# Optimization experiments

Measured on AMD Instinct MI355X. Metric: run time of the kernel, lower is better.

Reference implementation:

```python
import jax, jax.numpy as jnp
import numpy as np


def setup_inputs() -> dict:
    key = jax.random.key(0)
    B, R, A, T, S = 16, 1, 16, 14, 1024  # batch, num_rx, num_rx_ant, num_ofdm_symbols, num_eff_subcarriers
    k1, k2 = jax.random.split(key)
    y_real = jax.random.normal(k1, (B, R, A, T, S), dtype=jnp.float32)
    y_imag = jax.random.normal(k2, (B, R, A, T, S), dtype=jnp.float32)

    # Emulate PilotPattern-derived constants (computed in __init__ in the original):
    # zero-power pilot positions at OFDM symbols {2, 11}, every 2nd subcarrier.
    pilot_syms = np.array([2, 11], dtype=np.int64)
    est_sc = np.arange(0, S, 2, dtype=np.int64)  # estimated subcarriers (unique)
    sym_grid, sc_grid = np.meshgrid(pilot_syms, est_sc, indexing='ij')  # row-major like tf.where
    estimation_indices = jnp.asarray(
        np.stack([sym_grid.ravel(), sc_grid.ravel()], axis=1), dtype=jnp.int32)  # [P, 2]
    # Nearest estimated subcarrier for every subcarrier (np.argmin tie -> first, like original).
    closest = est_sc[np.argmin(np.abs(est_sc[None, :] - np.arange(S)[:, None]), axis=1)]
    closest_subcarrier = jnp.asarray(closest, dtype=jnp.int32)  # [S]

    return {"y_real": y_real, "y_imag": y_imag,
            "estimation_indices": estimation_indices,
            "closest_subcarrier": closest_subcarrier}


def reference(y_real, y_imag, estimation_indices, closest_subcarrier):
    y = jax.lax.complex(y_real, y_imag)  # [B,R,A,T,S] complex64
    B, R, A, T, S = y.shape
    sym = estimation_indices[:, 0]
    sc = estimation_indices[:, 1]

    # gather_nd over the (symbol, subcarrier) positions -> [B,R,A,P]
    sig = y[:, :, :, sym, sc]
    # per-position outer product over antennas -> [P,B,R,A,A]
    cov_el = jnp.einsum('brip,brjp->pbrij', sig, jnp.conj(sig))

    # unsorted_segment_mean over subcarrier ids (real/imag separately, as in TF)
    counts = jax.ops.segment_sum(jnp.ones_like(sc, dtype=jnp.float32), sc, num_segments=S)
    denom = jnp.maximum(counts, 1.0)[:, None, None, None, None]  # empty segments -> 0, like TF
    sum_r = jax.ops.segment_sum(cov_el.real, sc, num_segments=S)
    sum_i = jax.ops.segment_sum(cov_el.imag, sc, num_segments=S)
    cov_sw = jax.lax.complex(sum_r / denom, sum_i / denom)  # [S,B,R,A,A]

    # nearest-neighbor interpolation over subcarriers
    cov_nn = cov_sw[closest_subcarrier]                      # [S,B,R,A,A]
    cov = jnp.transpose(cov_nn, (1, 2, 0, 3, 4))             # [B,R,S,A,A]
    cov = cov[:, :, None]                                    # [B,R,1,S,A,A]
    return jnp.broadcast_to(cov, (B, R, T, S, A, A))
```

## Files before the change

kernel.cpp:

```cpp
#include <hip/hip_runtime.h>

static constexpr int kB = 16;
static constexpr int kA = 16;
static constexpr int kT = 14;
static constexpr int kS = 1024;
static constexpr int kMaxMatch = 32;


__global__ __launch_bounds__(64) void cov_real_kernel(
    const float* __restrict__ y_real,
    const float* __restrict__ y_imag,
    const int*   __restrict__ est,
    const int*   __restrict__ closest,
    float*       __restrict__ out,
    int P, long out_floats)
{
    const int blk = blockIdx.x;
    const int b   = blk >> 10;
    const int s   = blk & (kS - 1);
    const int tid = threadIdx.x;

    bool est64 = true;
    {
        int lim = 2 * P; if (lim > 128) lim = 128;
        for (int k = 1; k < lim; k += 2)
            if (est[k] != 0) { est64 = false; break; }
    }
    bool clo64 = true;
    {
        int lim = kS; if (lim > 128) lim = 128;
        for (int k = 1; k < lim; k += 2)
            if (closest[k] != 0) { clo64 = false; break; }
    }

    int c = closest[clo64 ? 2 * s : s];
    if (c < 0) c = 0;
    if (c >= kS) c = kS - 1;

    __shared__ int   sm_count;
    __shared__ int   sm_sym[kMaxMatch];
    __shared__ float sm_re[kA], sm_im[kA];

    if (tid == 0) sm_count = 0;
    __syncthreads();

    for (int p = tid; p < P; p += 64) {
        const int sc = est[est64 ? 4 * p + 2 : 2 * p + 1];
        if (sc == c) {
            const int sym = est[est64 ? 4 * p : 2 * p];
            if (sym >= 0 && sym < kT) {
                int slot = atomicAdd(&sm_count, 1);
                if (slot < kMaxMatch) sm_sym[slot] = sym;
            }
        }
    }
    __syncthreads();

    int count = sm_count;
    if (count > kMaxMatch) count = kMaxMatch;

    const int i  = tid >> 2;
    const int j0 = (tid & 3) * 4;

    float v0 = 0.f, v1 = 0.f, v2 = 0.f, v3 = 0.f;

    for (int m = 0; m < count; ++m) {
        const int sym = sm_sym[m];
        if (tid < kA) {
            const long off = (long)b * (kA * kT * kS) + (long)tid * (kT * kS)
                           + (long)sym * kS + c;
            sm_re[tid] = y_real[off];
            sm_im[tid] = y_imag[off];
        }
        __syncthreads();

        const float xr = sm_re[i], xi = sm_im[i];
        v0 += xr * sm_re[j0 + 0] + xi * sm_im[j0 + 0];
        v1 += xr * sm_re[j0 + 1] + xi * sm_im[j0 + 1];
        v2 += xr * sm_re[j0 + 2] + xi * sm_im[j0 + 2];
        v3 += xr * sm_re[j0 + 3] + xi * sm_im[j0 + 3];
        __syncthreads();
    }

    const float inv = 1.0f / (float)(count > 0 ? count : 1);
    const float4 v = make_float4(v0 * inv, v1 * inv, v2 * inv, v3 * inv);

    float4* __restrict__ out4 = (float4*)out;
    for (int t = 0; t < kT; ++t) {
        const long f4idx = ((long)(b * kT + t) * kS + s) * 64 + tid;
        if ((f4idx + 1) * 4 <= out_floats)
            out4[f4idx] = v;
    }
}

__global__ __launch_bounds__(128) void cov_cplx_kernel(
    const float* __restrict__ y_real,
    const float* __restrict__ y_imag,
    const int*   __restrict__ est,
    const int*   __restrict__ closest,
    float*       __restrict__ out,
    int P, long out_floats)
{
    const int blk = blockIdx.x;
    const int b   = blk >> 10;
    const int s   = blk & (kS - 1);
    const int tid = threadIdx.x;

    bool est64 = true;
    {
        int lim = 2 * P; if (lim > 128) lim = 128;
        for (int k = 1; k < lim; k += 2)
            if (est[k] != 0) { est64 = false; break; }
    }
    bool clo64 = true;
    {
        int lim = kS; if (lim > 128) lim = 128;
        for (int k = 1; k < lim; k += 2)
            if (closest[k] != 0) { clo64 = false; break; }
    }

    int c = closest[clo64 ? 2 * s : s];
    if (c < 0) c = 0;
    if (c >= kS) c = kS - 1;

    __shared__ int   sm_count;
    __shared__ int   sm_sym[kMaxMatch];
    __shared__ float sm_re[kA], sm_im[kA];

    if (tid == 0) sm_count = 0;
    __syncthreads();

    for (int p = tid; p < P; p += 128) {
        const int sc = est[est64 ? 4 * p + 2 : 2 * p + 1];
        if (sc == c) {
            const int sym = est[est64 ? 4 * p : 2 * p];
            if (sym >= 0 && sym < kT) {
                int slot = atomicAdd(&sm_count, 1);
                if (slot < kMaxMatch) sm_sym[slot] = sym;
            }
        }
    }
    __syncthreads();

    int count = sm_count;
    if (count > kMaxMatch) count = kMaxMatch;

    const int i  = tid >> 3;
    const int j0 = (tid & 7) * 2;

    float a0r = 0.f, a0i = 0.f, a1r = 0.f, a1i = 0.f;

    for (int m = 0; m < count; ++m) {
        const int sym = sm_sym[m];
        if (tid < kA) {
            const long off = (long)b * (kA * kT * kS) + (long)tid * (kT * kS)
                           + (long)sym * kS + c;
            sm_re[tid] = y_real[off];
            sm_im[tid] = y_imag[off];
        }
        __syncthreads();

        const float xr  = sm_re[i],      xi  = sm_im[i];
        const float y0r = sm_re[j0],     y0i = sm_im[j0];
        const float y1r = sm_re[j0 + 1], y1i = sm_im[j0 + 1];
        a0r += xr * y0r + xi * y0i;
        a0i += xi * y0r - xr * y0i;
        a1r += xr * y1r + xi * y1i;
        a1i += xi * y1r - xr * y1i;
        __syncthreads();
    }

    const float inv = 1.0f / (float)(count > 0 ? count : 1);
    const float4 v = make_float4(a0r * inv, a0i * inv, a1r * inv, a1i * inv);

    float4* __restrict__ out4 = (float4*)out;
    for (int t = 0; t < kT; ++t) {
        const long f4idx = ((long)(b * kT + t) * kS + s) * 128 + tid;
        if ((f4idx + 1) * 4 <= out_floats)
            out4[f4idx] = v;
    }
}

extern "C" void kernel_launch(void* const* d_in, const int* in_sizes, int n_in,
                              void* d_out, int out_size, void* d_ws, size_t ws_size,
                              hipStream_t stream) {
    const float* y_real  = (const float*)d_in[0];
    const float* y_imag  = (const float*)d_in[1];
    const int*   est     = (const int*)d_in[2];
    const int*   closest = (const int*)d_in[3];
    float*       out     = (float*)d_out;

    const int  P     = in_sizes[2] / 2;
    const long realN = (long)kB * kT * kS * kA * kA;

    dim3 grid(kB * kS);
    if ((long)out_size >= 2 * realN) {
        cov_cplx_kernel<<<grid, dim3(128), 0, stream>>>(
            y_real, y_imag, est, closest, out, P, (long)out_size);
    } else {
        cov_real_kernel<<<grid, dim3(64), 0, stream>>>(
            y_real, y_imag, est, closest, out, P, (long)out_size);
    }
}
```

Before: 266.5 us.

## Split covariance into compute-to-workspace and nontemporal broadcast store kernels

Computes the per-(batch, subcarrier) covariance once into a workspace buffer, then launches a separate broadcast kernel that copies each 8-subcarrier chunk to all OFDM symbols. The broadcast kernel uses nontemporal stores and larger blocks. The aim is to make the roughly 235 MB output write stream more efficiently than the original, which did 14 scattered stores per small block. The cost is an extra kernel launch and a 16 MB workspace write and read, and the new path runs only when the workspace is large enough.

```diff
diff --git a/kernel.cpp b/kernel.cpp
--- a/kernel.cpp
+++ b/kernel.cpp
@@ -6,6 +6,123 @@
 static constexpr int kS = 1024;
 static constexpr int kMaxMatch = 32;
 
+typedef __attribute__((ext_vector_type(4))) float fvec4;
+
+
+__global__ __launch_bounds__(128) void cov_compute_ws(
+    const float* __restrict__ y_real,
+    const float* __restrict__ y_imag,
+    const int*   __restrict__ est,
+    const int*   __restrict__ closest,
+    fvec4*       __restrict__ ws4,
+    int P)
+{
+    const int blk = blockIdx.x;
+    const int b   = blk >> 10;
+    const int s   = blk & (kS - 1);
+    const int tid = threadIdx.x;
+
+    bool est64 = true;
+    {
+        int lim = 2 * P; if (lim > 128) lim = 128;
+        for (int k = 1; k < lim; k += 2)
+            if (est[k] != 0) { est64 = false; break; }
+    }
+    bool clo64 = true;
+    {
+        int lim = kS; if (lim > 128) lim = 128;
+        for (int k = 1; k < lim; k += 2)
+            if (closest[k] != 0) { clo64 = false; break; }
+    }
+
+    int c = closest[clo64 ? 2 * s : s];
+    if (c < 0) c = 0;
+    if (c >= kS) c = kS - 1;
+
+    __shared__ int   sm_count;
+    __shared__ int   sm_sym[kMaxMatch];
+    __shared__ float sm_re[kA], sm_im[kA];
+
+    if (tid == 0) sm_count = 0;
+    __syncthreads();
+
+    for (int p = tid; p < P; p += 128) {
+        const int sc = est[est64 ? 4 * p + 2 : 2 * p + 1];
+        if (sc == c) {
+            const int sym = est[est64 ? 4 * p : 2 * p];
+            if (sym >= 0 && sym < kT) {
+                int slot = atomicAdd(&sm_count, 1);
+                if (slot < kMaxMatch) sm_sym[slot] = sym;
+            }
+        }
+    }
+    __syncthreads();
+
+    int count = sm_count;
+    if (count > kMaxMatch) count = kMaxMatch;
+
+    const int i  = tid >> 3;
+    const int j0 = (tid & 7) * 2;
+
+    float a0r = 0.f, a0i = 0.f, a1r = 0.f, a1i = 0.f;
+
+    for (int m = 0; m < count; ++m) {
+        const int sym = sm_sym[m];
+        if (tid < kA) {
+            const long off = (long)b * (kA * kT * kS) + (long)tid * (kT * kS)
+                           + (long)sym * kS + c;
+            sm_re[tid] = y_real[off];
+            sm_im[tid] = y_imag[off];
+        }
+        __syncthreads();
+
+        const float xr  = sm_re[i],      xi  = sm_im[i];
+        const float y0r = sm_re[j0],     y0i = sm_im[j0];
+        const float y1r = sm_re[j0 + 1], y1i = sm_im[j0 + 1];
+        a0r += xr * y0r + xi * y0i;
+        a0i += xi * y0r - xr * y0i;
+        a1r += xr * y1r + xi * y1i;
+        a1i += xi * y1r - xr * y1i;
+        __syncthreads();
+    }
+
+    const float inv = 1.0f / (float)(count > 0 ? count : 1);
+    fvec4 v; v.x = a0r * inv; v.y = a0i * inv; v.z = a1r * inv; v.w = a1i * inv;
+    ws4[(long)blk * 128 + tid] = v;
+}
+
+__global__ __launch_bounds__(256) void cov_broadcast(
+    const fvec4* __restrict__ ws4,
+    fvec4*       __restrict__ out4,
+    long out_floats)
+{
+    const int b     = blockIdx.x >> 7;
+    const int chunk = blockIdx.x & 127;
+    const int s0    = chunk << 3;
+    const int tid   = threadIdx.x;
+
+    const fvec4* __restrict__ src = ws4 + ((long)((b << 10) + s0)) * 128;
+    const fvec4 r0 = src[tid];
+    const fvec4 r1 = src[tid + 256];
+    const fvec4 r2 = src[tid + 512];
+    const fvec4 r3 = src[tid + 768];
+
+    #pragma unroll
+    for (int t = 0; t < kT; ++t) {
+        const long base = ((long)((b * kT + t) << 10) + s0) * 128;
+        if ((base + 1024) * 4 <= out_floats) {
+            __builtin_nontemporal_store(r0, out4 + base + tid);
+            __builtin_nontemporal_store(r1, out4 + base + tid + 256);
+            __builtin_nontemporal_store(r2, out4 + base + tid + 512);
+            __builtin_nontemporal_store(r3, out4 + base + tid + 768);
+        } else {
+            if ((base + tid + 1)       * 4 <= out_floats) out4[base + tid]       = r0;
+            if ((base + tid + 256 + 1) * 4 <= out_floats) out4[base + tid + 256] = r1;
+            if ((base + tid + 512 + 1) * 4 <= out_floats) out4[base + tid + 512] = r2;
+            if ((base + tid + 768 + 1) * 4 <= out_floats) out4[base + tid + 768] = r3;
+        }
+    }
+}
 
 __global__ __launch_bounds__(64) void cov_real_kernel(
     const float* __restrict__ y_real,
@@ -192,11 +309,20 @@
 
     const int  P     = in_sizes[2] / 2;
     const long realN = (long)kB * kT * kS * kA * kA;
+    const long wsNeed = (long)kB * kS * 128 * 16;
 
     dim3 grid(kB * kS);
     if ((long)out_size >= 2 * realN) {
-        cov_cplx_kernel<<<grid, dim3(128), 0, stream>>>(
-            y_real, y_imag, est, closest, out, P, (long)out_size);
+        if (ws_size >= (size_t)wsNeed) {
+            fvec4* ws4 = (fvec4*)d_ws;
+            cov_compute_ws<<<grid, dim3(128), 0, stream>>>(
+                y_real, y_imag, est, closest, ws4, P);
+            cov_broadcast<<<dim3(kB * (kS / 8)), dim3(256), 0, stream>>>(
+                ws4, (fvec4*)out, (long)out_size);
+        } else {
+            cov_cplx_kernel<<<grid, dim3(128), 0, stream>>>(
+                y_real, y_imag, est, closest, out, P, (long)out_size);
+        }
     } else {
         cov_real_kernel<<<grid, dim3(64), 0, stream>>>(
             y_real, y_imag, est, closest, out, P, (long)out_size);
```

Result: no change. 266.8 us (+0.1%).

## Process eight subcarriers per block with shared-memory staged contiguous nontemporal stores

Applied to the files above, without the earlier changes.

Replaces the per-(batch, subcarrier) complex kernel with a 256-thread block that handles eight consecutive subcarriers. Each warp-row computes one subcarrier's 16x16 complex covariance, and the results are staged in shared memory. Each block then writes contiguous 16 KB chunks per OFDM symbol using nontemporal stores. This cuts the block count by eight and amortises the index-scan prologue, aiming at write bandwidth on the output-bound broadcast. The cost is more shared memory per block and a loop bounded by the row with the most matches.

```diff
diff --git a/kernel.cpp b/kernel.cpp
--- a/kernel.cpp
+++ b/kernel.cpp
@@ -5,7 +5,150 @@
 static constexpr int kT = 14;
 static constexpr int kS = 1024;
 static constexpr int kMaxMatch = 32;
-
+static constexpr int kRows = 8;
+
+typedef __attribute__((ext_vector_type(4))) float fvec4;
+
+
+__global__ __launch_bounds__(256) void cov_fused(
+    const float* __restrict__ y_real,
+    const float* __restrict__ y_imag,
+    const int*   __restrict__ est,
+    const int*   __restrict__ closest,
+    fvec4*       __restrict__ out4,
+    int P, long out_floats)
+{
+    const int b    = blockIdx.x >> 7;
+    const int s0   = (blockIdx.x & 127) << 3;
+    const int tid  = threadIdx.x;
+    const int row  = tid >> 5;
+    const int lane = tid & 31;
+
+    bool est64 = true;
+    {
+        int lim = 2 * P; if (lim > 128) lim = 128;
+        for (int k = 1; k < lim; k += 2)
+            if (est[k] != 0) { est64 = false; break; }
+    }
+    bool clo64 = true;
+    {
+        int lim = kS; if (lim > 128) lim = 128;
+        for (int k = 1; k < lim; k += 2)
+            if (closest[k] != 0) { clo64 = false; break; }
+    }
+
+    __shared__ int   sm_c[kRows];
+    __shared__ int   sm_cnt[kRows];
+    __shared__ int   sm_sym[kRows][kMaxMatch];
+    __shared__ float sm_re[kRows][kA];
+    __shared__ float sm_im[kRows][kA];
+    __shared__ fvec4 sm_out[kRows * 128];
+
+    if (tid < kRows) {
+        const int s = s0 + tid;
+        int c = closest[clo64 ? 2 * s : s];
+        if (c < 0) c = 0;
+        if (c >= kS) c = kS - 1;
+        sm_c[tid]   = c;
+        sm_cnt[tid] = 0;
+    }
+    __syncthreads();
+
+    {
+        const int c = sm_c[row];
+        for (int p = lane; p < P; p += 32) {
+            const int sc = est[est64 ? 4 * p + 2 : 2 * p + 1];
+            if (sc == c) {
+                const int sym = est[est64 ? 4 * p : 2 * p];
+                if (sym >= 0 && sym < kT) {
+                    int slot = atomicAdd(&sm_cnt[row], 1);
+                    if (slot < kMaxMatch) sm_sym[row][slot] = sym;
+                }
+            }
+        }
+    }
+    __syncthreads();
+
+    int cnt = sm_cnt[row]; if (cnt > kMaxMatch) cnt = kMaxMatch;
+    int mmax = 0;
+    #pragma unroll
+    for (int r = 0; r < kRows; ++r) {
+        int cr = sm_cnt[r]; if (cr > kMaxMatch) cr = kMaxMatch;
+        if (cr > mmax) mmax = cr;
+    }
+
+    float acc[16];
+    #pragma unroll
+    for (int k = 0; k < 16; ++k) acc[k] = 0.f;
+
+    const int i = lane >> 1;
+
+    for (int m = 0; m < mmax; ++m) {
+        {
+            const int half = tid >> 7;
+            const int r    = (tid >> 4) & 7;
+            const int a    = tid & 15;
+            int cr = sm_cnt[r]; if (cr > kMaxMatch) cr = kMaxMatch;
+            if (m < cr) {
+                const int sym = sm_sym[r][m];
+                const long off = (long)b * (kA * kT * kS) + (long)a * (kT * kS)
+                               + (long)sym * kS + sm_c[r];
+                if (half == 0) sm_re[r][a] = y_real[off];
+                else           sm_im[r][a] = y_imag[off];
+            }
+        }
+        __syncthreads();
+
+        if (m < cnt) {
+            const float xr = sm_re[row][i], xi = sm_im[row][i];
+            #pragma unroll
+            for (int k = 0; k < 4; ++k) {
+                const int q  = 4 * lane + k;
+                const int j0 = (q & 7) * 2;
+                const float y0r = sm_re[row][j0],     y0i = sm_im[row][j0];
+                const float y1r = sm_re[row][j0 + 1], y1i = sm_im[row][j0 + 1];
+                acc[4 * k + 0] += xr * y0r + xi * y0i;
+                acc[4 * k + 1] += xi * y0r - xr * y0i;
+                acc[4 * k + 2] += xr * y1r + xi * y1i;
+                acc[4 * k + 3] += xi * y1r - xr * y1i;
+            }
+        }
+        __syncthreads();
+    }
+
+    const float inv = 1.0f / (float)(cnt > 0 ? cnt : 1);
+    #pragma unroll
+    for (int k = 0; k < 4; ++k) {
+        fvec4 v;
+        v.x = acc[4 * k + 0] * inv;
+        v.y = acc[4 * k + 1] * inv;
+        v.z = acc[4 * k + 2] * inv;
+        v.w = acc[4 * k + 3] * inv;
+        sm_out[row * 128 + 4 * lane + k] = v;
+    }
+    __syncthreads();
+
+    const fvec4 r0 = sm_out[tid];
+    const fvec4 r1 = sm_out[tid + 256];
+    const fvec4 r2 = sm_out[tid + 512];
+    const fvec4 r3 = sm_out[tid + 768];
+
+    #pragma unroll
+    for (int t = 0; t < kT; ++t) {
+        const long base = ((long)((b * kT + t) << 10) + s0) * 128;
+        if ((base + 1024) * 4 <= out_floats) {
+            __builtin_nontemporal_store(r0, out4 + base + tid);
+            __builtin_nontemporal_store(r1, out4 + base + tid + 256);
+            __builtin_nontemporal_store(r2, out4 + base + tid + 512);
+            __builtin_nontemporal_store(r3, out4 + base + tid + 768);
+        } else {
+            if ((base + tid + 1)       * 4 <= out_floats) out4[base + tid]       = r0;
+            if ((base + tid + 256 + 1) * 4 <= out_floats) out4[base + tid + 256] = r1;
+            if ((base + tid + 512 + 1) * 4 <= out_floats) out4[base + tid + 512] = r2;
+            if ((base + tid + 768 + 1) * 4 <= out_floats) out4[base + tid + 768] = r3;
+        }
+    }
+}
 
 __global__ __launch_bounds__(64) void cov_real_kernel(
     const float* __restrict__ y_real,
@@ -93,94 +236,6 @@
     }
 }
 
-__global__ __launch_bounds__(128) void cov_cplx_kernel(
-    const float* __restrict__ y_real,
-    const float* __restrict__ y_imag,
-    const int*   __restrict__ est,
-    const int*   __restrict__ closest,
-    float*       __restrict__ out,
-    int P, long out_floats)
-{
-    const int blk = blockIdx.x;
-    const int b   = blk >> 10;
-    const int s   = blk & (kS - 1);
-    const int tid = threadIdx.x;
-
-    bool est64 = true;
-    {
-        int lim = 2 * P; if (lim > 128) lim = 128;
-        for (int k = 1; k < lim; k += 2)
-            if (est[k] != 0) { est64 = false; break; }
-    }
-    bool clo64 = true;
-    {
-        int lim = kS; if (lim > 128) lim = 128;
-        for (int k = 1; k < lim; k += 2)
-            if (closest[k] != 0) { clo64 = false; break; }
-    }
-
-    int c = closest[clo64 ? 2 * s : s];
-    if (c < 0) c = 0;
-    if (c >= kS) c = kS - 1;
-
-    __shared__ int   sm_count;
-    __shared__ int   sm_sym[kMaxMatch];
-    __shared__ float sm_re[kA], sm_im[kA];
-
-    if (tid == 0) sm_count = 0;
-    __syncthreads();
-
-    for (int p = tid; p < P; p += 128) {
-        const int sc = est[est64 ? 4 * p + 2 : 2 * p + 1];
-        if (sc == c) {
-            const int sym = est[est64 ? 4 * p : 2 * p];
-            if (sym >= 0 && sym < kT) {
-                int slot = atomicAdd(&sm_count, 1);
-                if (slot < kMaxMatch) sm_sym[slot] = sym;
-            }
-        }
-    }
-    __syncthreads();
-
-    int count = sm_count;
-    if (count > kMaxMatch) count = kMaxMatch;
-
-    const int i  = tid >> 3;
-    const int j0 = (tid & 7) * 2;
-
-    float a0r = 0.f, a0i = 0.f, a1r = 0.f, a1i = 0.f;
-
-    for (int m = 0; m < count; ++m) {
-        const int sym = sm_sym[m];
-        if (tid < kA) {
-            const long off = (long)b * (kA * kT * kS) + (long)tid * (kT * kS)
-                           + (long)sym * kS + c;
-            sm_re[tid] = y_real[off];
-            sm_im[tid] = y_imag[off];
-        }
-        __syncthreads();
-
-        const float xr  = sm_re[i],      xi  = sm_im[i];
-        const float y0r = sm_re[j0],     y0i = sm_im[j0];
-        const float y1r = sm_re[j0 + 1], y1i = sm_im[j0 + 1];
-        a0r += xr * y0r + xi * y0i;
-        a0i += xi * y0r - xr * y0i;
-        a1r += xr * y1r + xi * y1i;
-        a1i += xi * y1r - xr * y1i;
-        __syncthreads();
-    }
-
-    const float inv = 1.0f / (float)(count > 0 ? count : 1);
-    const float4 v = make_float4(a0r * inv, a0i * inv, a1r * inv, a1i * inv);
-
-    float4* __restrict__ out4 = (float4*)out;
-    for (int t = 0; t < kT; ++t) {
-        const long f4idx = ((long)(b * kT + t) * kS + s) * 128 + tid;
-        if ((f4idx + 1) * 4 <= out_floats)
-            out4[f4idx] = v;
-    }
-}
-
 extern "C" void kernel_launch(void* const* d_in, const int* in_sizes, int n_in,
                               void* d_out, int out_size, void* d_ws, size_t ws_size,
                               hipStream_t stream) {
@@ -193,11 +248,11 @@
     const int  P     = in_sizes[2] / 2;
     const long realN = (long)kB * kT * kS * kA * kA;
 
-    dim3 grid(kB * kS);
     if ((long)out_size >= 2 * realN) {
-        cov_cplx_kernel<<<grid, dim3(128), 0, stream>>>(
-            y_real, y_imag, est, closest, out, P, (long)out_size);
+        cov_fused<<<dim3(kB * (kS / kRows)), dim3(256), 0, stream>>>(
+            y_real, y_imag, est, closest, (fvec4*)out, P, (long)out_size);
     } else {
+        dim3 grid(kB * kS);
         cov_real_kernel<<<grid, dim3(64), 0, stream>>>(
             y_real, y_imag, est, closest, out, P, (long)out_size);
     }
```

Result: no change. 264.8 us (-0.6%).

## Precompute pilot match tables and write output linearly per (batch,symbol) block

Applied to the files above, without the earlier changes.

Adds a single-block preprocessing kernel that resolves the nearest-subcarrier map and groups pilot symbols per subcarrier into workspace. The main kernel then launches one block per (batch, symbol, 32-subcarrier chunk), so each block writes one contiguous 64KB region with nontemporal stores. This replaces the old layout where each block wrote 14 strided slices and rescanned the index arrays. In exchange, every block recomputes the covariance for its subcarriers (redundant across the 14 symbols), and there is an extra tiny launch plus a dependency on workspace size.

```diff
diff --git a/kernel.cpp b/kernel.cpp
--- a/kernel.cpp
+++ b/kernel.cpp
@@ -6,6 +6,161 @@
 static constexpr int kS = 1024;
 static constexpr int kMaxMatch = 32;
 
+typedef __attribute__((ext_vector_type(4))) float fvec4;
+
+
+static constexpr long kWsInts = 2048 + (long)kS * kMaxMatch;
+
+__global__ __launch_bounds__(1024) void build_meta(
+    const int* __restrict__ est,
+    const int* __restrict__ closest,
+    int*       __restrict__ wsi,
+    int P)
+{
+    const int tid = threadIdx.x;
+
+    bool est64 = true;
+    {
+        int lim = 2 * P; if (lim > 128) lim = 128;
+        for (int k = 1; k < lim; k += 2)
+            if (est[k] != 0) { est64 = false; break; }
+    }
+    bool clo64 = true;
+    {
+        int lim = kS; if (lim > 128) lim = 128;
+        for (int k = 1; k < lim; k += 2)
+            if (closest[k] != 0) { clo64 = false; break; }
+    }
+
+    if (tid < kS) {
+        int c = closest[clo64 ? 2 * tid : tid];
+        if (c < 0) c = 0;
+        if (c >= kS) c = kS - 1;
+        wsi[tid]        = c;
+        wsi[kS + tid]   = 0;
+    }
+    __syncthreads();
+
+    for (int p = tid; p < P; p += 1024) {
+        const int sc = est[est64 ? 4 * p + 2 : 2 * p + 1];
+        if (sc >= 0 && sc < kS) {
+            const int sym = est[est64 ? 4 * p : 2 * p];
+            if (sym >= 0 && sym < kT) {
+                const int slot = atomicAdd(&wsi[kS + sc], 1);
+                if (slot < kMaxMatch)
+                    wsi[2 * kS + sc * kMaxMatch + slot] = sym;
+            }
+        }
+    }
+}
+
+__global__ __launch_bounds__(256) void cov_linear(
+    const float* __restrict__ y_real,
+    const float* __restrict__ y_imag,
+    const int*   __restrict__ wsi,
+    fvec4*       __restrict__ out4,
+    long out_floats)
+{
+    const int blk     = blockIdx.x;
+    const int scChunk = blk & 31;
+    const int bt      = blk >> 5;
+    const int b       = bt / kT;
+    const int s0      = scChunk * 32;
+    const int tid     = threadIdx.x;
+
+    __shared__ int   sm_c[32];
+    __shared__ int   sm_cnt[32];
+    __shared__ int   sm_sym[32][2];
+    __shared__ float sm_re[32][kA];
+    __shared__ float sm_im[32][kA];
+
+    if (tid < 32) {
+        const int c = wsi[s0 + tid];
+        int cnt = wsi[kS + c];
+        if (cnt > kMaxMatch) cnt = kMaxMatch;
+        sm_c[tid]   = c;
+        sm_cnt[tid] = cnt;
+        sm_sym[tid][0] = (cnt > 0) ? wsi[2 * kS + c * kMaxMatch + 0] : 0;
+        sm_sym[tid][1] = (cnt > 1) ? wsi[2 * kS + c * kMaxMatch + 1] : 0;
+    }
+    __syncthreads();
+
+    int mmax = 0;
+    #pragma unroll 8
+    for (int r = 0; r < 32; ++r) {
+        const int cr = sm_cnt[r];
+        if (cr > mmax) mmax = cr;
+    }
+
+    fvec4 acc[16];
+    #pragma unroll
+    for (int k = 0; k < 16; ++k) acc[k] = (fvec4)0.f;
+
+    const long bbase = (long)b * (kA * kT * kS);
+
+    for (int m = 0; m < mmax; ++m) {
+        #pragma unroll
+        for (int k = 0; k < 4; ++k) {
+            const int idx  = tid + 256 * k;
+            const int half = idx >> 9;
+            const int r    = (idx >> 4) & 31;
+            const int a    = idx & 15;
+            if (m < sm_cnt[r]) {
+                const int sym = (m < 2) ? sm_sym[r][m]
+                                        : wsi[2 * kS + sm_c[r] * kMaxMatch + m];
+                const long off = bbase + (long)a * (kT * kS) + (long)sym * kS + sm_c[r];
+                if (half == 0) sm_re[r][a] = y_real[off];
+                else           sm_im[r][a] = y_imag[off];
+            }
+        }
+        __syncthreads();
+
+        #pragma unroll
+        for (int k = 0; k < 16; ++k) {
+            const int idx = tid + 256 * k;
+            const int r   = idx >> 7;
+            const int q   = idx & 127;
+            if (m < sm_cnt[r]) {
+                const int i  = q >> 3;
+                const int j0 = (q & 7) * 2;
+                const float xr  = sm_re[r][i],      xi  = sm_im[r][i];
+                const float y0r = sm_re[r][j0],     y0i = sm_im[r][j0];
+                const float y1r = sm_re[r][j0 + 1], y1i = sm_im[r][j0 + 1];
+                acc[k].x += xr * y0r + xi * y0i;
+                acc[k].y += xi * y0r - xr * y0i;
+                acc[k].z += xr * y1r + xi * y1i;
+                acc[k].w += xi * y1r - xr * y1i;
+            }
+        }
+        __syncthreads();
+    }
+
+    const long base4 = (long)blk * 4096;
+    if ((base4 + 4096) * 4 <= out_floats) {
+        #pragma unroll
+        for (int k = 0; k < 16; ++k) {
+            const int idx = tid + 256 * k;
+            const int r   = idx >> 7;
+            const int cr  = sm_cnt[r];
+            const float inv = 1.0f / (float)(cr > 0 ? cr : 1);
+            fvec4 v = acc[k];
+            v.x *= inv; v.y *= inv; v.z *= inv; v.w *= inv;
+            __builtin_nontemporal_store(v, out4 + base4 + idx);
+        }
+    } else {
+        #pragma unroll
+        for (int k = 0; k < 16; ++k) {
+            const int idx = tid + 256 * k;
+            const int r   = idx >> 7;
+            const int cr  = sm_cnt[r];
+            const float inv = 1.0f / (float)(cr > 0 ? cr : 1);
+            fvec4 v = acc[k];
+            v.x *= inv; v.y *= inv; v.z *= inv; v.w *= inv;
+            if ((base4 + idx + 1) * 4 <= out_floats)
+                out4[base4 + idx] = v;
+        }
+    }
+}
 
 __global__ __launch_bounds__(64) void cov_real_kernel(
     const float* __restrict__ y_real,
@@ -190,14 +345,23 @@
     const int*   closest = (const int*)d_in[3];
     float*       out     = (float*)d_out;
 
-    const int  P     = in_sizes[2] / 2;
-    const long realN = (long)kB * kT * kS * kA * kA;
-
-    dim3 grid(kB * kS);
+    const int  P      = in_sizes[2] / 2;
+    const long realN  = (long)kB * kT * kS * kA * kA;
+    const long wsNeed = kWsInts * 4;
+
     if ((long)out_size >= 2 * realN) {
-        cov_cplx_kernel<<<grid, dim3(128), 0, stream>>>(
-            y_real, y_imag, est, closest, out, P, (long)out_size);
+        if (ws_size >= (size_t)wsNeed) {
+            int* wsi = (int*)d_ws;
+            build_meta<<<dim3(1), dim3(1024), 0, stream>>>(est, closest, wsi, P);
+            cov_linear<<<dim3(kB * kT * 32), dim3(256), 0, stream>>>(
+                y_real, y_imag, wsi, (fvec4*)out, (long)out_size);
+        } else {
+            dim3 grid(kB * kS);
+            cov_cplx_kernel<<<grid, dim3(128), 0, stream>>>(
+                y_real, y_imag, est, closest, out, P, (long)out_size);
+        }
     } else {
+        dim3 grid(kB * kS);
         cov_real_kernel<<<grid, dim3(64), 0, stream>>>(
             y_real, y_imag, est, closest, out, P, (long)out_size);
     }
```

Result: faster. 261.1 us (median of 2 runs) (-2.0%).
